# Kernel optimization log

Hardware: AMD Instinct MI355X
Metric: run time of the kernel (lower is better)

## Reference

```python
import jax, jax.numpy as jnp
import numpy as np

N_NODES = 100000
N_EDGES = 100000
D = 256
N_SIDE = 2  # rel_list = [side_a, side_b, rel_c, rel_d]
N_REL = 2


def setup_inputs() -> dict:
    key = jax.random.key(0)
    ks = jax.random.split(key, 7)
    h = jax.random.normal(ks[0], (N_NODES, D), dtype=jnp.float32)
    src_idx = jax.random.randint(ks[1], (N_SIDE + N_REL, N_EDGES), 0, N_NODES)
    dst_idx = jax.random.randint(ks[2], (N_SIDE + N_REL, N_EDGES), 0, N_NODES)
    # shared bilinear matrix R (nn.Linear(D, D, bias=False): y = x @ R_W.T)
    R_W = jax.random.normal(ks[3], (D, D), dtype=jnp.float32) * (1.0 / np.sqrt(D))
    # per-'side*' diagonal parameters (xavier over [D,1] then squeeze)
    d_side = jax.random.normal(ks[4], (N_SIDE, D), dtype=jnp.float32)
    # per-regular-relation Linear weights (with bias)
    W_rel = jax.random.normal(ks[5], (N_REL, D, D), dtype=jnp.float32) * (1.0 / np.sqrt(D))
    b_rel = jax.random.normal(ks[6], (N_REL, D), dtype=jnp.float32) * 0.01
    return {"h": h, "src_idx": src_idx, "dst_idx": dst_idx,
            "R_W": R_W, "d_side": d_side, "W_rel": W_rel, "b_rel": b_rel}


def reference(h, src_idx, dst_idx, R_W, d_side, W_rel, b_rel):
    # --- 'side*' edge types: score = (((h_u * d) @ R_W.T) * d) . h_v ---
    hu_s = h[src_idx[:N_SIDE]]            # [S, E, D] gather
    hv_s = h[dst_idx[:N_SIDE]]            # [S, E, D]
    lft = hu_s * d_side[:, None, :]       # [S, E, D]
    lft = jnp.einsum('sed,fd->sef', lft, R_W)  # Linear, no bias
    lft = lft * d_side[:, None, :]
    score_side = jnp.einsum('sed,sed->se', lft, hv_s)  # [S, E]

    # --- regular edge types: score = (h_u @ W.T + b) . h_v ---
    hu_r = h[src_idx[N_SIDE:]]            # [R, E, D]
    hv_r = h[dst_idx[N_SIDE:]]            # [R, E, D]
    lft_r = jnp.einsum('red,rfd->ref', hu_r, W_rel) + b_rel[:, None, :]
    score_rel = jnp.einsum('red,red->re', lft_r, hv_r)  # [R, E]

    return jnp.concatenate([score_side, score_rel], axis=0)  # [S+R, E]
```

## Files before the change

kernel.cpp:

```cpp
#include <hip/hip_runtime.h>
#include <stdint.h>

#define NNODES 100000
#define NEDGES 100000
#define DIM    256
#define NCH    4
#define ET     32
#define RSF    264

typedef _Float16 f16x8 __attribute__((ext_vector_type(8)));
typedef _Float16 f16x4 __attribute__((ext_vector_type(4)));
typedef float f32x4  __attribute__((ext_vector_type(4)));

__global__ void prep_fused(const float* __restrict__ RW,
                           const float* __restrict__ dside,
                           const float* __restrict__ Wrel,
                           const float* __restrict__ h,
                           _Float16* __restrict__ Bh, _Float16* __restrict__ Bl,
                           _Float16* __restrict__ H16) {
    if (blockIdx.x < 128) {
        int t = blockIdx.x * blockDim.x + threadIdx.x;
        int lane = t & 63;
        int ft   = (t >> 6) & 15;
        int kc   = (t >> 10) & 7;
        int c    = t >> 13;
        int quad = lane >> 4, col = lane & 15;
        int f     = ft * 16 + col;
        int kbase = kc * 32 + quad * 8;

        f16x8 vh, vl;
#pragma unroll
        for (int j = 0; j < 8; ++j) {
            int k = kbase + j;
            float val;
            if (c < 2) {
                val = dside[c * DIM + f] * RW[f * DIM + k] * dside[c * DIM + k];
            } else {
                val = Wrel[(size_t)(c - 2) * DIM * DIM + f * DIM + k];
            }
            _Float16 hi = (_Float16)val;
            vh[j] = hi;
            vl[j] = (_Float16)(val - (float)hi);
        }
        ((f16x8*)Bh)[t] = vh;
        ((f16x8*)Bl)[t] = vl;
    } else {
        int u = (blockIdx.x - 128) * blockDim.x + threadIdx.x;
        if (u >= NNODES * DIM / 8) return;
        f32x4 x0 = ((const f32x4*)h)[2 * u];
        f32x4 x1 = ((const f32x4*)h)[2 * u + 1];
        f16x8 o;
#pragma unroll
        for (int j = 0; j < 4; ++j) {
            o[j]     = (_Float16)x0[j];
            o[4 + j] = (_Float16)x1[j];
        }
        ((f16x8*)H16)[u] = o;
    }
}

__global__ __launch_bounds__(256, 2)
void edge_kernel(const _Float16* __restrict__ H16,
                 const int* __restrict__ src_idx,
                 const int* __restrict__ dst_idx,
                 const float* __restrict__ brel,
                 const _Float16* __restrict__ Bh_sw,
                 const _Float16* __restrict__ Bl_sw,
                 float* __restrict__ out) {
    const int c    = blockIdx.y;
    const int e0   = blockIdx.x * ET;
    const int tid  = threadIdx.x;
    const int w    = tid >> 6;
    const int lane = tid & 63;
    const int quad = lane >> 4, col = lane & 15;

    __shared__ __align__(16) _Float16 s_row[ET * RSF];
    __shared__ uint32_t s_src[ET];
    __shared__ uint32_t s_dst[ET];
    __shared__ float    red[4][ET];

    if (tid < ET) {
        int idx = e0 + tid;
        int si = 0, di = 0;
        if (idx < NEDGES) {
            si = src_idx[(size_t)c * NEDGES + idx];
            di = dst_idx[(size_t)c * NEDGES + idx];
        }
        s_src[tid] = (uint32_t)si;
        s_dst[tid] = (uint32_t)di;
    }
    __syncthreads();

#pragma unroll
    for (int i = 0; i < 8; ++i) {
        int lr = w * 8 + i;
        const _Float16* rb = H16 + (size_t)s_src[lr] * DIM;
        f16x4 x = *(const f16x4*)(rb + lane * 4);
        *(f16x4*)&s_row[lr * RSF + lane * 4] = x;
    }
    __syncthreads();

    f32x4 acc[2][4];
#pragma unroll
    for (int i = 0; i < 2; ++i)
#pragma unroll
        for (int j = 0; j < 4; ++j) acc[i][j] = (f32x4){0.f, 0.f, 0.f, 0.f};

    const f16x8* Bh = (const f16x8*)Bh_sw;
    const f16x8* Bl = (const f16x8*)Bl_sw;

#pragma unroll
    for (int kc = 0; kc < 8; ++kc) {
        f16x8 A[2];
#pragma unroll
        for (int mt = 0; mt < 2; ++mt)
            A[mt] = *(const f16x8*)&s_row[(mt * 16 + col) * RSF + kc * 32 + quad * 8];

        int fb = ((c * 8 + kc) * 16 + w * 4) * 64 + lane;
#pragma unroll
        for (int ft = 0; ft < 4; ++ft) {
            f16x8 bh = Bh[fb + ft * 64];
            f16x8 bl = Bl[fb + ft * 64];
#pragma unroll
            for (int mt = 0; mt < 2; ++mt) {
                acc[mt][ft] = __builtin_amdgcn_mfma_f32_16x16x32_f16(A[mt], bh, acc[mt][ft], 0, 0, 0);
                acc[mt][ft] = __builtin_amdgcn_mfma_f32_16x16x32_f16(A[mt], bl, acc[mt][ft], 0, 0, 0);
            }
        }
    }
    __syncthreads();

#pragma unroll
    for (int i = 0; i < 8; ++i) {
        int lr = w * 8 + i;
        const _Float16* rb = H16 + (size_t)s_dst[lr] * DIM;
        f16x4 x = *(const f16x4*)(rb + lane * 4);
        *(f16x4*)&s_row[lr * RSF + lane * 4] = x;
    }
    __syncthreads();

    float bias[4];
#pragma unroll
    for (int ft = 0; ft < 4; ++ft) {
        int f = w * 64 + ft * 16 + col;
        bias[ft] = (c >= 2) ? brel[(size_t)(c - 2) * DIM + f] : 0.f;
    }

    float psum[2][4];
#pragma unroll
    for (int mt = 0; mt < 2; ++mt) {
#pragma unroll
        for (int r = 0; r < 4; ++r) {
            int el = mt * 16 + quad * 4 + r;
            float s = 0.f;
#pragma unroll
            for (int ft = 0; ft < 4; ++ft) {
                int f = w * 64 + ft * 16 + col;
                float v = (float)s_row[el * RSF + f];
                s += (acc[mt][ft][r] + bias[ft]) * v;
            }
            psum[mt][r] = s;
        }
    }

#pragma unroll
    for (int off = 1; off < 16; off <<= 1) {
#pragma unroll
        for (int mt = 0; mt < 2; ++mt)
#pragma unroll
            for (int r = 0; r < 4; ++r)
                psum[mt][r] += __shfl_xor(psum[mt][r], off, 64);
    }
    if (col == 0) {
#pragma unroll
        for (int mt = 0; mt < 2; ++mt)
#pragma unroll
            for (int r = 0; r < 4; ++r)
                red[w][mt * 16 + quad * 4 + r] = psum[mt][r];
    }
    __syncthreads();

    if (tid < ET) {
        int idx = e0 + tid;
        if (idx < NEDGES) {
            float s = red[0][tid] + red[1][tid] + red[2][tid] + red[3][tid];
            out[(size_t)c * NEDGES + idx] = s;
        }
    }
}

extern "C" void kernel_launch(void* const* d_in, const int* in_sizes, int n_in,
                              void* d_out, int out_size, void* d_ws, size_t ws_size,
                              hipStream_t stream) {
    const float* hmat  = (const float*)d_in[0];
    const int*   src   = (const int*)d_in[1];
    const int*   dst   = (const int*)d_in[2];
    const float* RW    = (const float*)d_in[3];
    const float* dside = (const float*)d_in[4];
    const float* Wrel  = (const float*)d_in[5];
    const float* brel  = (const float*)d_in[6];
    float* out = (float*)d_out;

    const size_t nB = (size_t)NCH * DIM * DIM;
    _Float16* Bh  = (_Float16*)d_ws;
    _Float16* Bl  = Bh + nB;
    _Float16* H16 = Bl + nB;

    const int convBlocks = (NNODES * DIM / 8 + 255) / 256;
    prep_fused<<<dim3(128 + convBlocks), dim3(256), 0, stream>>>(
        RW, dside, Wrel, hmat, Bh, Bl, H16);

    dim3 grid((NEDGES + ET - 1) / ET, NCH);
    edge_kernel<<<grid, dim3(256), 0, stream>>>(H16, src, dst, brel, Bh, Bl, out);
}
```

Measured before the change: 314.7 us.

## Double edge tile to 64 with 512 threads, prefetch dst rows, grid-stride conversion

Edge tile grows from 32 to 64 edges per block and threads from 256 to 512, so each weight fragment loaded from global is reused across four M-tiles instead of two, halving B-matrix traffic per edge. Source and destination row gathers are both issued into registers up front, so the destination gather latency overlaps the MFMA phase. The fp32-to-fp16 conversion of h switches to a fixed 2048-block grid-stride loop with four independent loads per iteration. Costs are higher register pressure from holding prefetched rows and more accumulators, plus fewer blocks in flight.

```diff
diff --git a/kernel.cpp b/kernel.cpp
--- a/kernel.cpp
+++ b/kernel.cpp
@@ -5,8 +5,9 @@
 #define NEDGES 100000
 #define DIM    256
 #define NCH    4
-#define ET     32
+#define ET     64
 #define RSF    264
+#define CONVB  2048
 
 typedef _Float16 f16x8 __attribute__((ext_vector_type(8)));
 typedef _Float16 f16x4 __attribute__((ext_vector_type(4)));
@@ -45,21 +46,36 @@
         ((f16x8*)Bh)[t] = vh;
         ((f16x8*)Bl)[t] = vl;
     } else {
-        int u = (blockIdx.x - 128) * blockDim.x + threadIdx.x;
-        if (u >= NNODES * DIM / 8) return;
-        f32x4 x0 = ((const f32x4*)h)[2 * u];
-        f32x4 x1 = ((const f32x4*)h)[2 * u + 1];
-        f16x8 o;
-#pragma unroll
-        for (int j = 0; j < 4; ++j) {
-            o[j]     = (_Float16)x0[j];
-            o[4 + j] = (_Float16)x1[j];
-        }
-        ((f16x8*)H16)[u] = o;
+        const int total4 = NNODES * DIM / 4;
+        const int stride = CONVB * 256;
+        int i = (blockIdx.x - 128) * 256 + (int)threadIdx.x;
+        const f32x4* s4 = (const f32x4*)h;
+        f16x4* d4 = (f16x4*)H16;
+        for (; i + 3 * stride < total4; i += 4 * stride) {
+            f32x4 a  = s4[i];
+            f32x4 b  = s4[i + stride];
+            f32x4 cc = s4[i + 2 * stride];
+            f32x4 d  = s4[i + 3 * stride];
+            f16x4 oa, ob, oc, od;
+#pragma unroll
+            for (int j = 0; j < 4; ++j) {
+                oa[j] = (_Float16)a[j];  ob[j] = (_Float16)b[j];
+                oc[j] = (_Float16)cc[j]; od[j] = (_Float16)d[j];
+            }
+            d4[i] = oa; d4[i + stride] = ob;
+            d4[i + 2 * stride] = oc; d4[i + 3 * stride] = od;
+        }
+        for (; i < total4; i += stride) {
+            f32x4 a = s4[i];
+            f16x4 o;
+#pragma unroll
+            for (int j = 0; j < 4; ++j) o[j] = (_Float16)a[j];
+            d4[i] = o;
+        }
     }
 }
 
-__global__ __launch_bounds__(256, 2)
+__global__ __launch_bounds__(512, 2)
 void edge_kernel(const _Float16* __restrict__ H16,
                  const int* __restrict__ src_idx,
                  const int* __restrict__ dst_idx,
@@ -77,7 +93,7 @@
     __shared__ __align__(16) _Float16 s_row[ET * RSF];
     __shared__ uint32_t s_src[ET];
     __shared__ uint32_t s_dst[ET];
-    __shared__ float    red[4][ET];
+    __shared__ float    red[8][ET];
 
     if (tid < ET) {
         int idx = e0 + tid;
@@ -91,38 +107,47 @@
     }
     __syncthreads();
 
-#pragma unroll
-    for (int i = 0; i < 8; ++i) {
-        int lr = w * 8 + i;
-        const _Float16* rb = H16 + (size_t)s_src[lr] * DIM;
-        f16x4 x = *(const f16x4*)(rb + lane * 4);
-        *(f16x4*)&s_row[lr * RSF + lane * 4] = x;
-    }
-    __syncthreads();
-
-    f32x4 acc[2][4];
-#pragma unroll
-    for (int i = 0; i < 2; ++i)
-#pragma unroll
-        for (int j = 0; j < 4; ++j) acc[i][j] = (f32x4){0.f, 0.f, 0.f, 0.f};
+    f16x4 aR[8], vR[8];
+#pragma unroll
+    for (int i = 0; i < 8; ++i) {
+        int lr = w * 8 + i;
+        aR[i] = *(const f16x4*)(H16 + (size_t)s_src[lr] * DIM + lane * 4);
+    }
+#pragma unroll
+    for (int i = 0; i < 8; ++i) {
+        int lr = w * 8 + i;
+        vR[i] = *(const f16x4*)(H16 + (size_t)s_dst[lr] * DIM + lane * 4);
+    }
+#pragma unroll
+    for (int i = 0; i < 8; ++i) {
+        int lr = w * 8 + i;
+        *(f16x4*)&s_row[lr * RSF + lane * 4] = aR[i];
+    }
+    __syncthreads();
+
+    f32x4 acc[4][2];
+#pragma unroll
+    for (int mt = 0; mt < 4; ++mt)
+#pragma unroll
+        for (int ft = 0; ft < 2; ++ft) acc[mt][ft] = (f32x4){0.f, 0.f, 0.f, 0.f};
 
     const f16x8* Bh = (const f16x8*)Bh_sw;
     const f16x8* Bl = (const f16x8*)Bl_sw;
 
 #pragma unroll
     for (int kc = 0; kc < 8; ++kc) {
-        f16x8 A[2];
-#pragma unroll
-        for (int mt = 0; mt < 2; ++mt)
+        f16x8 A[4];
+#pragma unroll
+        for (int mt = 0; mt < 4; ++mt)
             A[mt] = *(const f16x8*)&s_row[(mt * 16 + col) * RSF + kc * 32 + quad * 8];
 
-        int fb = ((c * 8 + kc) * 16 + w * 4) * 64 + lane;
-#pragma unroll
-        for (int ft = 0; ft < 4; ++ft) {
+        int fb = ((c * 8 + kc) * 16 + w * 2) * 64 + lane;
+#pragma unroll
+        for (int ft = 0; ft < 2; ++ft) {
             f16x8 bh = Bh[fb + ft * 64];
             f16x8 bl = Bl[fb + ft * 64];
 #pragma unroll
-            for (int mt = 0; mt < 2; ++mt) {
+            for (int mt = 0; mt < 4; ++mt) {
                 acc[mt][ft] = __builtin_amdgcn_mfma_f32_16x16x32_f16(A[mt], bh, acc[mt][ft], 0, 0, 0);
                 acc[mt][ft] = __builtin_amdgcn_mfma_f32_16x16x32_f16(A[mt], bl, acc[mt][ft], 0, 0, 0);
             }
@@ -133,29 +158,27 @@
 #pragma unroll
     for (int i = 0; i < 8; ++i) {
         int lr = w * 8 + i;
-        const _Float16* rb = H16 + (size_t)s_dst[lr] * DIM;
-        f16x4 x = *(const f16x4*)(rb + lane * 4);
-        *(f16x4*)&s_row[lr * RSF + lane * 4] = x;
-    }
-    __syncthreads();
-
-    float bias[4];
-#pragma unroll
-    for (int ft = 0; ft < 4; ++ft) {
-        int f = w * 64 + ft * 16 + col;
+        *(f16x4*)&s_row[lr * RSF + lane * 4] = vR[i];
+    }
+    __syncthreads();
+
+    float bias[2];
+#pragma unroll
+    for (int ft = 0; ft < 2; ++ft) {
+        int f = w * 32 + ft * 16 + col;
         bias[ft] = (c >= 2) ? brel[(size_t)(c - 2) * DIM + f] : 0.f;
     }
 
-    float psum[2][4];
-#pragma unroll
-    for (int mt = 0; mt < 2; ++mt) {
+    float psum[4][4];
+#pragma unroll
+    for (int mt = 0; mt < 4; ++mt) {
 #pragma unroll
         for (int r = 0; r < 4; ++r) {
             int el = mt * 16 + quad * 4 + r;
             float s = 0.f;
 #pragma unroll
-            for (int ft = 0; ft < 4; ++ft) {
-                int f = w * 64 + ft * 16 + col;
+            for (int ft = 0; ft < 2; ++ft) {
+                int f = w * 32 + ft * 16 + col;
                 float v = (float)s_row[el * RSF + f];
                 s += (acc[mt][ft][r] + bias[ft]) * v;
             }
@@ -166,14 +189,14 @@
 #pragma unroll
     for (int off = 1; off < 16; off <<= 1) {
 #pragma unroll
-        for (int mt = 0; mt < 2; ++mt)
+        for (int mt = 0; mt < 4; ++mt)
 #pragma unroll
             for (int r = 0; r < 4; ++r)
                 psum[mt][r] += __shfl_xor(psum[mt][r], off, 64);
     }
     if (col == 0) {
 #pragma unroll
-        for (int mt = 0; mt < 2; ++mt)
+        for (int mt = 0; mt < 4; ++mt)
 #pragma unroll
             for (int r = 0; r < 4; ++r)
                 red[w][mt * 16 + quad * 4 + r] = psum[mt][r];
@@ -183,7 +206,9 @@
     if (tid < ET) {
         int idx = e0 + tid;
         if (idx < NEDGES) {
-            float s = red[0][tid] + red[1][tid] + red[2][tid] + red[3][tid];
+            float s = 0.f;
+#pragma unroll
+            for (int i = 0; i < 8; ++i) s += red[i][tid];
             out[(size_t)c * NEDGES + idx] = s;
         }
     }
@@ -206,10 +231,9 @@
     _Float16* Bl  = Bh + nB;
     _Float16* H16 = Bl + nB;
 
-    const int convBlocks = (NNODES * DIM / 8 + 255) / 256;
-    prep_fused<<<dim3(128 + convBlocks), dim3(256), 0, stream>>>(
+    prep_fused<<<dim3(128 + CONVB), dim3(256), 0, stream>>>(
         RW, dside, Wrel, hmat, Bh, Bl, H16);
 
     dim3 grid((NEDGES + ET - 1) / ET, NCH);
-    edge_kernel<<<grid, dim3(256), 0, stream>>>(H16, src, dst, brel, Bh, Bl, out);
+    edge_kernel<<<grid, dim3(512), 0, stream>>>(H16, src, dst, brel, Bh, Bl, out);
 }
```

Result: slower. 339.1 us (+7.7%).
